# Kernel optimization log

Hardware: AMD Instinct MI355X
Metric: run time of the kernel (lower is better)

Reference implementation:

```python
import jax, jax.numpy as jnp
import numpy as np

H1 = 36
H2 = 1


def _lstm(x, W_ih, W_hh, b_ih, b_hh, H):
    # x: [B, T, D]; W_ih: [4H, D]; W_hh: [4H, H]; biases: [4H]
    # PyTorch gate order: i, f, g, o
    B, T, _ = x.shape
    xg = jnp.einsum('btd,gd->btg', x, W_ih) + (b_ih + b_hh)  # [B, T, 4H]

    def step(carry, xg_t):
        h, c = carry
        g = xg_t + h @ W_hh.T  # [B, 4H]
        i, f, gc, o = jnp.split(g, 4, axis=-1)
        c = jax.nn.sigmoid(f) * c + jax.nn.sigmoid(i) * jnp.tanh(gc)
        h = jax.nn.sigmoid(o) * jnp.tanh(c)
        return (h, c), h

    h0 = jnp.zeros((B, H), x.dtype)
    (_, _), hs = jax.lax.scan(step, (h0, h0), jnp.swapaxes(xg, 0, 1))
    return jnp.swapaxes(hs, 0, 1)  # [B, T, H]


def setup_inputs() -> dict:
    key = jax.random.key(0)
    ks = jax.random.split(key, 9)
    B, T = 2048, 2048
    s1 = 1.0 / np.sqrt(H1)
    s2 = 1.0  # 1/sqrt(hidden_size=1)
    return {
        'x': jax.random.normal(ks[0], (B, T, 1), dtype=jnp.float32),
        'W_ih1': jax.random.uniform(ks[1], (4 * H1, 1), jnp.float32, -s1, s1),
        'W_hh1': jax.random.uniform(ks[2], (4 * H1, H1), jnp.float32, -s1, s1),
        'b_ih1': jax.random.uniform(ks[3], (4 * H1,), jnp.float32, -s1, s1),
        'b_hh1': jax.random.uniform(ks[4], (4 * H1,), jnp.float32, -s1, s1),
        'W_ih2': jax.random.uniform(ks[5], (4 * H2, H1), jnp.float32, -s2, s2),
        'W_hh2': jax.random.uniform(ks[6], (4 * H2, H2), jnp.float32, -s2, s2),
        'b_ih2': jax.random.uniform(ks[7], (4 * H2,), jnp.float32, -s2, s2),
        'b_hh2': jax.random.uniform(ks[8], (4 * H2,), jnp.float32, -s2, s2),
    }


def reference(x, W_ih1, W_hh1, b_ih1, b_hh1, W_ih2, W_hh2, b_ih2, b_hh2):
    h1 = _lstm(x, W_ih1, W_hh1, b_ih1, b_hh1, H1)   # [B, T, 36]
    h1 = jax.nn.relu(h1)
    out = _lstm(h1, W_ih2, W_hh2, b_ih2, b_hh2, H2)  # [B, T, 1]
    return out
```

## Files before the change

### kernel.cpp

```cpp
#include <hip/hip_runtime.h>

namespace {

constexpr int T_LEN = 2048;
constexpr int B_TOT = 2048;
constexpr int H1 = 36;
constexpr int NB = 16;
constexpr int BLOCK = 640;
constexpr int RS = 80;

typedef _Float16 f16x8 __attribute__((ext_vector_type(8)));
typedef _Float16 h16x2 __attribute__((ext_vector_type(2)));
typedef float f32x4 __attribute__((ext_vector_type(4)));

__device__ __forceinline__ float fdot2(float wb, float hb, float acc) {
#if __has_builtin(__builtin_amdgcn_fdot2)
  return __builtin_amdgcn_fdot2(__builtin_bit_cast(h16x2, wb),
                                __builtin_bit_cast(h16x2, hb), acc, false);
#else
  float d;
  asm("v_dot2_f32_f16 %0, %1, %2, %3" : "=v"(d) : "v"(wb), "v"(hb), "0"(acc));
  return d;
#endif
}
__device__ __forceinline__ float pack2h(float a, float b) {
  h16x2 t = {(_Float16)a, (_Float16)b};
  return __builtin_bit_cast(float, t);
}
template <int PAT>
__device__ __forceinline__ float swzf(float v) {
  return __builtin_bit_cast(
      float, __builtin_amdgcn_ds_swizzle(__builtin_bit_cast(int, v), PAT));
}
__device__ __forceinline__ float fexp2(float x) { return __builtin_amdgcn_exp2f(x); }
__device__ __forceinline__ float frcp(float x) { return __builtin_amdgcn_rcpf(x); }
__device__ __forceinline__ float sigm(float x) { return frcp(1.f + fexp2(x * -1.44269504f)); }
__device__ __forceinline__ float tanh_fast(float x) {
  return fmaf(2.f, frcp(1.f + fexp2(x * -2.88539008f)), -1.f);
}

__global__ __launch_bounds__(BLOCK) void lstm2_kernel(
    const float* __restrict__ x, const float* __restrict__ Wih1,
    const float* __restrict__ Whh1, const float* __restrict__ bih1,
    const float* __restrict__ bhh1, const float* __restrict__ Wih2,
    const float* __restrict__ Whh2, const float* __restrict__ bih2,
    const float* __restrict__ bhh2, float* __restrict__ out)
{
  __shared__ __align__(16) _Float16 lds[2][2][NB][RS];

  const int tid = threadIdx.x;
  const int wid = tid >> 6;
  const int lane = tid & 63;
  const int g0 = blockIdx.x * NB;
  const bool isA = wid < 9;

  for (int i = tid; i < 2 * 2 * NB * RS; i += BLOCK)
    ((_Float16*)lds)[i] = (_Float16)0.f;
  __syncthreads();

  const int m = lane & 15;
  const int q = lane >> 4;
  f16x8 A0 = {}, A1 = {};
  float wxc[4] = {0, 0, 0, 0}, bxc[4] = {0, 0, 0, 0};
  float c1 = 0.f;
  const float* xc = nullptr;
  if (isA) {
    const int u0 = wid * 4;
    const int ra = (m & 3) * H1 + (u0 + (m >> 2));
#pragma unroll
    for (int j = 0; j < 8; ++j) {
      A0[j] = (_Float16)Whh1[ra * H1 + q * 8 + j];
      const int k1 = 32 + q * 8 + j;
      A1[j] = (k1 < H1) ? (_Float16)Whh1[ra * H1 + k1] : (_Float16)0.f;
    }
#pragma unroll
    for (int r = 0; r < 4; ++r) {
      const int rc = r * H1 + (u0 + q);
      wxc[r] = Wih1[rc];
      bxc[r] = bih1[rc] + bhh1[rc];
    }
    xc = x + (size_t)(g0 + m) * T_LEN;
  }

  const int lb = lane >> 2, lg = lane & 3;
  float w2[18];
  float whg = 0.f, b2 = 0.f, c2 = 0.f, h2 = 0.f;
  float* outp = nullptr;
#pragma unroll
  for (int k = 0; k < 18; ++k) w2[k] = 0.f;
  if (!isA) {
    const float* wr = Wih2 + lg * H1;
#pragma unroll
    for (int k = 0; k < 18; ++k) w2[k] = pack2h(wr[2 * k], wr[2 * k + 1]);
    whg = Whh2[lg];
    b2 = bih2[lg] + bhh2[lg];
    outp = out + (size_t)(g0 + lb) * T_LEN;
  }

  float4 qx = make_float4(0.f, 0.f, 0.f, 0.f);
  if (isA) qx = *(const float4*)xc;
  float4 ov = make_float4(0.f, 0.f, 0.f, 0.f);

  auto step = [&](int i, float xv, int s) {
    const int ib = (s + 1) & 1;
    const int wb = s & 1;
    if (isA) {
      const f16x8 B0 = *(const f16x8*)&lds[ib][0][m][q * 8];
      const f16x8 B1 = *(const f16x8*)&lds[ib][0][m][32 + q * 8];
      f32x4 cc;
#pragma unroll
      for (int r = 0; r < 4; ++r) cc[r] = fmaf(xv, wxc[r], bxc[r]);
      cc = __builtin_amdgcn_mfma_f32_16x16x32_f16(A0, B0, cc, 0, 0, 0);
      cc = __builtin_amdgcn_mfma_f32_16x16x32_f16(A1, B1, cc, 0, 0, 0);
      const float I = sigm(cc[0]), F = sigm(cc[1]);
      const float G = tanh_fast(cc[2]), O = sigm(cc[3]);
      c1 = fmaf(F, c1, I * G);
      const float h = O * tanh_fast(c1);
      const int ku = (wid << 2) + q;
      lds[wb][0][m][ku] = (_Float16)h;
      lds[wb][1][m][ku] = (_Float16)fmaxf(h, 0.f);
    } else if (i > 0) {
      const char* rp = (const char*)&lds[ib][1][lb][0];
      const float4 r0 = *(const float4*)rp;
      const float4 r1 = *(const float4*)(rp + 16);
      const float4 r2 = *(const float4*)(rp + 32);
      const float4 r3 = *(const float4*)(rp + 48);
      const float2 r4 = *(const float2*)(rp + 64);
      const float f[18] = {r0.x, r0.y, r0.z, r0.w, r1.x, r1.y, r1.z, r1.w,
                           r2.x, r2.y, r2.z, r2.w, r3.x, r3.y, r3.z, r3.w,
                           r4.x, r4.y};
      float aE = 0.f, aO = 0.f;
#pragma unroll
      for (int k = 0; k < 18; k += 2) aE = fdot2(w2[k], f[k], aE);
#pragma unroll
      for (int k = 1; k < 18; k += 2) aO = fdot2(w2[k], f[k], aO);
      const float pre = (aE + aO) + fmaf(h2, whg, b2);
      const float pI = swzf<0x8000 | 0x00>(pre);
      const float pF = swzf<0x8000 | 0x55>(pre);
      const float pG = swzf<0x8000 | 0xAA>(pre);
      const float pO = swzf<0x8000 | 0xFF>(pre);
      c2 = fmaf(sigm(pF), c2, sigm(pI) * tanh_fast(pG));
      h2 = sigm(pO) * tanh_fast(c2);
      if (s == 1) ov.x = h2;
      else if (s == 2) ov.y = h2;
      else if (s == 3) ov.z = h2;
      else {
        ov.w = h2;
        if (lg == 0) *(float4*)(outp + (i - 4)) = ov;
      }
    }
    __syncthreads();
  };

  for (int i0 = 0; i0 < T_LEN; i0 += 4) {
    float4 qn = qx;
    if (isA) {
      const int tn = (i0 + 4 < T_LEN) ? (i0 + 4) : (T_LEN - 4);
      qn = *(const float4*)(xc + tn);
    }
    step(i0 + 0, qx.x, 0);
    step(i0 + 1, qx.y, 1);
    step(i0 + 2, qx.z, 2);
    step(i0 + 3, qx.w, 3);
    qx = qn;
  }
  step(T_LEN, qx.x, 0);
}

}

extern "C" void kernel_launch(void* const* d_in, const int* in_sizes, int n_in,
                              void* d_out, int out_size, void* d_ws, size_t ws_size,
                              hipStream_t stream) {
  const float* x    = (const float*)d_in[0];
  const float* Wih1 = (const float*)d_in[1];
  const float* Whh1 = (const float*)d_in[2];
  const float* bih1 = (const float*)d_in[3];
  const float* bhh1 = (const float*)d_in[4];
  const float* Wih2 = (const float*)d_in[5];
  const float* Whh2 = (const float*)d_in[6];
  const float* bih2 = (const float*)d_in[7];
  const float* bhh2 = (const float*)d_in[8];
  float* out = (float*)d_out;

  dim3 grid(B_TOT / NB);
  dim3 block(BLOCK);
  hipLaunchKernelGGL(lstm2_kernel, grid, block, 0, stream,
                     x, Wih1, Whh1, bih1, bhh1, Wih2, Whh2, bih2, bhh2, out);
}
```

Before: 907.1 us.

## Run both LSTM layers in a single wavefront per 16-sequence group without LDS

Replaces the 10-wave block, which used LDS double buffering and a barrier per timestep, with one 64-lane wave that computes all 36 hidden units through 18 MFMAs. The hidden state is fed back through registers, and the x input and bias are folded into the MFMA B operand as f16 hi/lo splits. Gate pre-activations are pre-scaled by the log2e factors so that sigmoid and tanh reduce to exp2 plus rcp. Layer 2 is computed in the same wave using dot2 and cross-lane swizzle/bpermute reductions. This removes all __syncthreads and LDS traffic, but it serialises the MFMA and transcendental work onto a single wave per group, giving much less parallelism per CU and a long per-step dependency chain.

```diff
diff --git a/kernel.cpp b/kernel.cpp
--- a/kernel.cpp
+++ b/kernel.cpp
@@ -6,8 +6,7 @@
 constexpr int B_TOT = 2048;
 constexpr int H1 = 36;
 constexpr int NB = 16;
-constexpr int BLOCK = 640;
-constexpr int RS = 80;
+constexpr int BLOCK = 64;
 
 typedef _Float16 f16x8 __attribute__((ext_vector_type(8)));
 typedef _Float16 h16x2 __attribute__((ext_vector_type(2)));
@@ -27,16 +26,34 @@
   h16x2 t = {(_Float16)a, (_Float16)b};
   return __builtin_bit_cast(float, t);
 }
-template <int PAT>
-__device__ __forceinline__ float swzf(float v) {
-  return __builtin_bit_cast(
-      float, __builtin_amdgcn_ds_swizzle(__builtin_bit_cast(int, v), PAT));
+__device__ __forceinline__ float pkrelu(float v) {
+  float r;
+  asm("v_pk_max_f16 %0, %1, %2" : "=v"(r) : "v"(v), "v"(0.f));
+  return r;
 }
 __device__ __forceinline__ float fexp2(float x) { return __builtin_amdgcn_exp2f(x); }
 __device__ __forceinline__ float frcp(float x) { return __builtin_amdgcn_rcpf(x); }
-__device__ __forceinline__ float sigm(float x) { return frcp(1.f + fexp2(x * -1.44269504f)); }
-__device__ __forceinline__ float tanh_fast(float x) {
-  return fmaf(2.f, frcp(1.f + fexp2(x * -2.88539008f)), -1.f);
+
+__device__ __forceinline__ float xl16(float v) {
+  return __builtin_bit_cast(
+      float, __builtin_amdgcn_ds_swizzle(__builtin_bit_cast(int, v), 0x401F));
+}
+__device__ __forceinline__ float xl32(float v, int lane) {
+  return __builtin_bit_cast(
+      float, __builtin_amdgcn_ds_bpermute((lane ^ 32) << 2,
+                                          __builtin_bit_cast(int, v)));
+}
+
+__device__ __forceinline__ float lstm_unit(float pi, float pf, float pg, float po,
+                                           float& cS) {
+  const float I = frcp(1.f + fexp2(pi));
+  const float F = frcp(1.f + fexp2(pf));
+  const float O = frcp(1.f + fexp2(po));
+  const float rG = frcp(1.f + fexp2(pg));
+  const float Gs = fmaf(rG, -5.77078016f, 2.88539008f);
+  cS = fmaf(F, cS, I * Gs);
+  const float rC = frcp(1.f + fexp2(cS));
+  return fmaf(rC, O + O, -O);
 }
 
 __global__ __launch_bounds__(BLOCK) void lstm2_kernel(
@@ -46,125 +63,127 @@
     const float* __restrict__ Whh2, const float* __restrict__ bih2,
     const float* __restrict__ bhh2, float* __restrict__ out)
 {
-  __shared__ __align__(16) _Float16 lds[2][2][NB][RS];
-
-  const int tid = threadIdx.x;
-  const int wid = tid >> 6;
-  const int lane = tid & 63;
-  const int g0 = blockIdx.x * NB;
-  const bool isA = wid < 9;
-
-  for (int i = tid; i < 2 * 2 * NB * RS; i += BLOCK)
-    ((_Float16*)lds)[i] = (_Float16)0.f;
-  __syncthreads();
-
+  const int lane = threadIdx.x & 63;
   const int m = lane & 15;
   const int q = lane >> 4;
-  f16x8 A0 = {}, A1 = {};
-  float wxc[4] = {0, 0, 0, 0}, bxc[4] = {0, 0, 0, 0};
-  float c1 = 0.f;
-  const float* xc = nullptr;
-  if (isA) {
-    const int u0 = wid * 4;
-    const int ra = (m & 3) * H1 + (u0 + (m >> 2));
-#pragma unroll
-    for (int j = 0; j < 8; ++j) {
-      A0[j] = (_Float16)Whh1[ra * H1 + q * 8 + j];
-      const int k1 = 32 + q * 8 + j;
-      A1[j] = (k1 < H1) ? (_Float16)Whh1[ra * H1 + k1] : (_Float16)0.f;
+  const int g0 = blockIdx.x * NB;
+
+  const int ga = m & 3;
+  const int qa = m >> 2;
+  const float sga = (ga == 2) ? -2.88539008f : -1.44269504f;
+
+  f16x8 A0[9], A1[9];
+#pragma unroll
+  for (int t = 0; t < 9; ++t) {
+    const int uA = (t < 8) ? (8 * qa + t) : (32 + qa);
+    const int row = ga * H1 + uA;
+#pragma unroll
+    for (int j = 0; j < 8; ++j)
+      A0[t][j] = (_Float16)(sga * Whh1[row * H1 + q * 8 + j]);
+#pragma unroll
+    for (int j = 0; j < 8; ++j) A1[t][j] = (_Float16)0.f;
+    A1[t][0] = (_Float16)(sga * Whh1[row * H1 + 32 + q]);
+    if (q == 0) {
+      const _Float16 wih = (_Float16)(sga * Wih1[row]);
+      A1[t][1] = wih;
+      A1[t][2] = wih;
+      const float bb = sga * (bih1[row] + bhh1[row]);
+      const _Float16 bh = (_Float16)bb;
+      A1[t][3] = bh;
+      A1[t][4] = (_Float16)(bb - (float)bh);
     }
-#pragma unroll
-    for (int r = 0; r < 4; ++r) {
-      const int rc = r * H1 + (u0 + q);
-      wxc[r] = Wih1[rc];
-      bxc[r] = bih1[rc] + bhh1[rc];
+  }
+
+  float w2p[4][4], w2s[4], whg2[4], b2s[4];
+#pragma unroll
+  for (int g2 = 0; g2 < 4; ++g2) {
+    const float s2 = (g2 == 2) ? -2.88539008f : -1.44269504f;
+    const float* wr = Wih2 + g2 * H1;
+#pragma unroll
+    for (int d = 0; d < 4; ++d)
+      w2p[g2][d] = pack2h(s2 * wr[8 * q + 2 * d], s2 * wr[8 * q + 2 * d + 1]);
+    w2s[g2] = s2 * wr[32 + q];
+    whg2[g2] = s2 * Whh2[g2];
+    b2s[g2] = s2 * (bih2[g2] + bhh2[g2]);
+  }
+
+  float cS[9];
+#pragma unroll
+  for (int t = 0; t < 9; ++t) cS[t] = 0.f;
+  float c2S = 0.f, h2 = 0.f;
+
+  f16x8 B0, B1;
+#pragma unroll
+  for (int j = 0; j < 8; ++j) { B0[j] = (_Float16)0.f; B1[j] = (_Float16)0.f; }
+  B1[3] = (_Float16)1.f;
+  B1[4] = (_Float16)1.f;
+
+  const float* xc = x + (size_t)(g0 + m) * T_LEN;
+  float* outp = out + (size_t)(g0 + m) * T_LEN;
+  float4 qx = *(const float4*)xc;
+  float4 ov = make_float4(0.f, 0.f, 0.f, 0.f);
+
+  const f32x4 z4 = {0.f, 0.f, 0.f, 0.f};
+
+  auto step = [&](int i, float xv, int s) {
+    const _Float16 xh = (_Float16)xv;
+    B1[1] = xh;
+    B1[2] = (_Float16)(xv - (float)xh);
+
+    f32x4 cc[9];
+#pragma unroll
+    for (int t = 0; t < 9; ++t)
+      cc[t] = __builtin_amdgcn_mfma_f32_16x16x32_f16(A0[t], B0, z4, 0, 0, 0);
+#pragma unroll
+    for (int t = 0; t < 9; ++t)
+      cc[t] = __builtin_amdgcn_mfma_f32_16x16x32_f16(A1[t], B1, cc[t], 0, 0, 0);
+
+    float h[9];
+#pragma unroll
+    for (int t = 0; t < 9; ++t)
+      h[t] = lstm_unit(cc[t][0], cc[t][1], cc[t][2], cc[t][3], cS[t]);
+
+#pragma unroll
+    for (int t = 0; t < 8; ++t) B0[t] = (_Float16)h[t];
+    B1[0] = (_Float16)h[8];
+
+    const f32x4 b0d = __builtin_bit_cast(f32x4, B0);
+    float pk[4];
+#pragma unroll
+    for (int d = 0; d < 4; ++d) pk[d] = pkrelu(b0d[d]);
+    const float rl8 = fmaxf(h[8], 0.f);
+    float pre[4];
+#pragma unroll
+    for (int g2 = 0; g2 < 4; ++g2) {
+      float aE = fdot2(w2p[g2][0], pk[0], rl8 * w2s[g2]);
+      float aO = fdot2(w2p[g2][1], pk[1], 0.f);
+      aE = fdot2(w2p[g2][2], pk[2], aE);
+      aO = fdot2(w2p[g2][3], pk[3], aO);
+      float p = aE + aO;
+      p += xl16(p);
+      p += xl32(p, lane);
+      pre[g2] = fmaf(h2, whg2[g2], p + b2s[g2]);
     }
-    xc = x + (size_t)(g0 + m) * T_LEN;
-  }
-
-  const int lb = lane >> 2, lg = lane & 3;
-  float w2[18];
-  float whg = 0.f, b2 = 0.f, c2 = 0.f, h2 = 0.f;
-  float* outp = nullptr;
-#pragma unroll
-  for (int k = 0; k < 18; ++k) w2[k] = 0.f;
-  if (!isA) {
-    const float* wr = Wih2 + lg * H1;
-#pragma unroll
-    for (int k = 0; k < 18; ++k) w2[k] = pack2h(wr[2 * k], wr[2 * k + 1]);
-    whg = Whh2[lg];
-    b2 = bih2[lg] + bhh2[lg];
-    outp = out + (size_t)(g0 + lb) * T_LEN;
-  }
-
-  float4 qx = make_float4(0.f, 0.f, 0.f, 0.f);
-  if (isA) qx = *(const float4*)xc;
-  float4 ov = make_float4(0.f, 0.f, 0.f, 0.f);
-
-  auto step = [&](int i, float xv, int s) {
-    const int ib = (s + 1) & 1;
-    const int wb = s & 1;
-    if (isA) {
-      const f16x8 B0 = *(const f16x8*)&lds[ib][0][m][q * 8];
-      const f16x8 B1 = *(const f16x8*)&lds[ib][0][m][32 + q * 8];
-      f32x4 cc;
-#pragma unroll
-      for (int r = 0; r < 4; ++r) cc[r] = fmaf(xv, wxc[r], bxc[r]);
-      cc = __builtin_amdgcn_mfma_f32_16x16x32_f16(A0, B0, cc, 0, 0, 0);
-      cc = __builtin_amdgcn_mfma_f32_16x16x32_f16(A1, B1, cc, 0, 0, 0);
-      const float I = sigm(cc[0]), F = sigm(cc[1]);
-      const float G = tanh_fast(cc[2]), O = sigm(cc[3]);
-      c1 = fmaf(F, c1, I * G);
-      const float h = O * tanh_fast(c1);
-      const int ku = (wid << 2) + q;
-      lds[wb][0][m][ku] = (_Float16)h;
-      lds[wb][1][m][ku] = (_Float16)fmaxf(h, 0.f);
-    } else if (i > 0) {
-      const char* rp = (const char*)&lds[ib][1][lb][0];
-      const float4 r0 = *(const float4*)rp;
-      const float4 r1 = *(const float4*)(rp + 16);
-      const float4 r2 = *(const float4*)(rp + 32);
-      const float4 r3 = *(const float4*)(rp + 48);
-      const float2 r4 = *(const float2*)(rp + 64);
-      const float f[18] = {r0.x, r0.y, r0.z, r0.w, r1.x, r1.y, r1.z, r1.w,
-                           r2.x, r2.y, r2.z, r2.w, r3.x, r3.y, r3.z, r3.w,
-                           r4.x, r4.y};
-      float aE = 0.f, aO = 0.f;
-#pragma unroll
-      for (int k = 0; k < 18; k += 2) aE = fdot2(w2[k], f[k], aE);
-#pragma unroll
-      for (int k = 1; k < 18; k += 2) aO = fdot2(w2[k], f[k], aO);
-      const float pre = (aE + aO) + fmaf(h2, whg, b2);
-      const float pI = swzf<0x8000 | 0x00>(pre);
-      const float pF = swzf<0x8000 | 0x55>(pre);
-      const float pG = swzf<0x8000 | 0xAA>(pre);
-      const float pO = swzf<0x8000 | 0xFF>(pre);
-      c2 = fmaf(sigm(pF), c2, sigm(pI) * tanh_fast(pG));
-      h2 = sigm(pO) * tanh_fast(c2);
-      if (s == 1) ov.x = h2;
-      else if (s == 2) ov.y = h2;
-      else if (s == 3) ov.z = h2;
-      else {
-        ov.w = h2;
-        if (lg == 0) *(float4*)(outp + (i - 4)) = ov;
-      }
+    h2 = lstm_unit(pre[0], pre[1], pre[2], pre[3], c2S);
+
+    if (s == 0) ov.x = h2;
+    else if (s == 1) ov.y = h2;
+    else if (s == 2) ov.z = h2;
+    else {
+      ov.w = h2;
+      if (q == 0) *(float4*)(outp + (i - 3)) = ov;
     }
-    __syncthreads();
   };
 
   for (int i0 = 0; i0 < T_LEN; i0 += 4) {
-    float4 qn = qx;
-    if (isA) {
-      const int tn = (i0 + 4 < T_LEN) ? (i0 + 4) : (T_LEN - 4);
-      qn = *(const float4*)(xc + tn);
-    }
+    const int tn = (i0 + 4 < T_LEN) ? (i0 + 4) : (T_LEN - 4);
+    const float4 qn = *(const float4*)(xc + tn);
     step(i0 + 0, qx.x, 0);
     step(i0 + 1, qx.y, 1);
     step(i0 + 2, qx.z, 2);
     step(i0 + 3, qx.w, 3);
     qx = qn;
   }
-  step(T_LEN, qx.x, 0);
 }
 
 }
```

Result: slower. 1.865 ms (+105.6%).
